# Performance work log

Hardware: AMD Instinct MI355X
Metric: run time of the kernel (lower is better)

## Reference

```python
import jax, jax.numpy as jnp
import numpy as np

B, SL, D, E, STEPS = 8, 1024, 128, 4, 5


def setup_inputs() -> dict:
    key = jax.random.key(0)
    ks = jax.random.split(key, 13)
    s = 0.02  # xavier-ish init scale
    return {
        "batchinput": jax.random.normal(ks[0], (B, SL, D), jnp.float32),
        # dense per-edge-type adjacency [B, sl, sl*E]; scaled so bmm output stays O(1)
        "batchgraphin": jax.random.uniform(ks[1], (B, SL, SL * E), jnp.float32) / SL,
        "batchgraphout": jax.random.uniform(ks[2], (B, SL, SL * E), jnp.float32) / SL,
        "W_in": jax.random.normal(ks[3], (E * D, E * D), jnp.float32) * s,
        "b_in": jnp.zeros((E * D,), jnp.float32),
        "W_out": jax.random.normal(ks[4], (E * D, E * D), jnp.float32) * s,
        "b_out": jnp.zeros((E * D,), jnp.float32),
        "W_r": jax.random.normal(ks[5], (D, 3 * D), jnp.float32) * s,
        "b_r": jnp.zeros((D,), jnp.float32),
        "W_z": jax.random.normal(ks[6], (D, 3 * D), jnp.float32) * s,
        "b_z": jnp.zeros((D,), jnp.float32),
        "W_t": jax.random.normal(ks[7], (D, 3 * D), jnp.float32) * s,
        "b_t": jnp.zeros((D,), jnp.float32),
    }


def reference(batchinput, batchgraphin, batchgraphout,
              W_in, b_in, W_out, b_out,
              W_r, b_r, W_z, b_z, W_t, b_t):
    out = batchinput  # [B, SL, D]
    for _ in range(STEPS):
        # tile node state across edge types: [B, SL, E*D]
        temp = jnp.broadcast_to(out[:, :, None, :], (B, SL, E, D)).reshape(B, SL, E * D)
        gi = (temp @ W_in.T + b_in).reshape(B, SL * E, D)
        gi = jnp.einsum('bse,bed->bsd', batchgraphin, gi)   # [B, SL, D]
        go = (temp @ W_out.T + b_out).reshape(B, SL * E, D)
        go = jnp.einsum('bse,bed->bsd', batchgraphout, go)  # [B, SL, D]
        # GRU-style gated update
        cat = jnp.concatenate([gi, go, out], axis=-1)       # [B, SL, 3D]
        r = jax.nn.sigmoid(cat @ W_r.T + b_r)
        z = jax.nn.sigmoid(cat @ W_z.T + b_z)
        h_hat = jnp.tanh(jnp.concatenate([gi, go, r * out], axis=-1) @ W_t.T + b_t)
        out = (1.0 - z) * out + z * h_hat
    return out
```

## Files before the change

### kernel.cpp

```cpp
#include <hip/hip_runtime.h>
#include <cstdint>
#include <cstddef>


typedef unsigned short u16;
typedef unsigned int u32;
typedef float f32x4 __attribute__((ext_vector_type(4)));
typedef short short8 __attribute__((ext_vector_type(8)));
typedef u16 u16x4 __attribute__((ext_vector_type(4)));
typedef u16 u16x8 __attribute__((ext_vector_type(8)));

__device__ __forceinline__ float b2f(u16 h) {
  union { u32 u; float f; } v; v.u = ((u32)h) << 16; return v.f;
}
__device__ __forceinline__ u16 f2bf(float f) {
  union { float f; u32 u; } v; v.f = f;
  u32 r = (v.u + 0x7fffu + ((v.u >> 16) & 1u)) >> 16;
  return (u16)r;
}
__device__ __forceinline__ float ldu(const void* p, size_t i, int flag) {
  return flag ? ((const float*)p)[i] : b2f(((const u16*)p)[i]);
}
__device__ __forceinline__ void gload_lds16(const void* g, void* l) {
  __builtin_amdgcn_global_load_lds((const __attribute__((address_space(1))) void*)g,
                                   (__attribute__((address_space(3))) void*)l,
                                   16, 0, 0);
}

__global__ void k_detect(const u16* g, int* flag) {
  __shared__ int bad;
  if (threadIdx.x == 0) bad = 0;
  __syncthreads();
  int any = 0;
  for (int i = threadIdx.x; i < 8192; i += 256) any |= (g[i] > 0x3B00);
  if (any) atomicOr(&bad, 1);
  __syncthreads();
  if (threadIdx.x == 0) *flag = bad;
}

__global__ void k_cvtf(const void* src, float* dst, int n, const int* flagp) {
  int i = blockIdx.x * 256 + threadIdx.x;
  if (i < n) dst[i] = ldu(src, i, *flagp);
}

__global__ void k_weff(const void* Win, const void* bin, const void* Wout, const void* bout,
                       u16* weffHT, u16* weffLT, float* biasf, const int* flagp) {
  int flag = *flagp;
  int idx = blockIdx.x * 256 + threadIdx.x;
  int j = idx >> 7, k = idx & 127;
  float s = 0.f;
  if (j < 512) {
#pragma unroll
    for (int e = 0; e < 4; e++) s += ldu(Win, (size_t)j * 512 + e * 128 + k, flag);
  } else {
#pragma unroll
    for (int e = 0; e < 4; e++) s += ldu(Wout, (size_t)(j - 512) * 512 + e * 128 + k, flag);
  }
  u16 h = f2bf(s);
  weffHT[(size_t)j * 128 + k] = h;
  weffLT[(size_t)j * 128 + k] = f2bf(s - b2f(h));
  if (idx < 1024) biasf[idx] = (idx < 512) ? ldu(bin, idx, flag) : ldu(bout, idx - 512, flag);
}

__global__ void k_wt3(const void* Wr, const void* Wz, const void* Wt,
                      const void* br, const void* bz, const void* bt,
                      u16* wt3H, u16* wt3L,
                      float* brf, float* bzf, float* btf, const int* flagp) {
  int flag = *flagp;
  int idx = blockIdx.x * 256 + threadIdx.x;
  int g = idx / 49152, rem = idx % 49152;
  const void* W = (g == 0) ? Wr : (g == 1) ? Wz : Wt;
  float s = ldu(W, rem, flag);
  u16 h = f2bf(s);
  wt3H[(size_t)idx] = h;
  wt3L[(size_t)idx] = f2bf(s - b2f(h));
  if (rem < 128) {
    float bv = ldu((g == 0) ? br : (g == 1) ? bz : bt, rem, flag);
    ((g == 0) ? brf : (g == 1) ? bzf : btf)[rem] = bv;
  }
}

__global__ __launch_bounds__(512, 2) void kg_pre_mfma(
    const u16* __restrict__ weffHT, const u16* __restrict__ weffLT,
    const float* __restrict__ biasf, const float* __restrict__ outF,
    u16* __restrict__ gpreT) {
  __shared__ __align__(16) u16 AH[32 * 128];
  __shared__ __align__(16) u16 AL[32 * 128];
  __shared__ __align__(16) u16 ybuf[32 * 1024];
  int t = threadIdx.x;
  int b = blockIdx.y;
  int s0 = blockIdx.x * 32;
  {
    int row = t >> 4, c8 = (t & 15) * 8;
    const float* src = outF + (((size_t)(b * 1024 + s0 + row)) << 7) + c8;
    f32x4 x0 = *(const f32x4*)src;
    f32x4 x1 = *(const f32x4*)(src + 4);
    u16x8 vh, vl;
#pragma unroll
    for (int i = 0; i < 4; i++) {
      float x = x0[i]; u16 h = f2bf(x);
      vh[i] = h; vl[i] = f2bf(x - b2f(h));
      x = x1[i]; h = f2bf(x);
      vh[i + 4] = h; vl[i + 4] = f2bf(x - b2f(h));
    }
    int bc = (c8 * 2) ^ ((row & 7) << 4);
    *(u16x8*)((char*)AH + row * 256 + bc) = vh;
    *(u16x8*)((char*)AL + row * 256 + bc) = vl;
  }
  __syncthreads();
  int lane = t & 63, w = t >> 6;
  int wm = w >> 2, wn = w & 3;
  int lr = lane & 15, lk = lane >> 4;
  int n0 = wn * 256;
  int arow = wm * 16 + lr;
  int abase_row = arow * 256;
  int aswz = (arow & 7) << 4;
  f32x4 acc[16] = {};
#pragma unroll
  for (int kk = 0; kk < 4; kk++) {
    int kb = (kk * 64 + lk * 16) ^ aswz;
    short8 ah = *(const short8*)((const char*)AH + abase_row + kb);
    short8 al = *(const short8*)((const char*)AL + abase_row + kb);
    int wko = kk * 64 + lk * 16;
#pragma unroll
    for (int nf = 0; nf < 16; nf++) {
      int j = n0 + nf * 16 + lr;
      short8 wh = *(const short8*)((const char*)weffHT + (size_t)j * 256 + wko);
      short8 wl = *(const short8*)((const char*)weffLT + (size_t)j * 256 + wko);
      acc[nf] = __builtin_amdgcn_mfma_f32_16x16x32_bf16(ah, wh, acc[nf], 0, 0, 0);
      acc[nf] = __builtin_amdgcn_mfma_f32_16x16x32_bf16(ah, wl, acc[nf], 0, 0, 0);
      acc[nf] = __builtin_amdgcn_mfma_f32_16x16x32_bf16(al, wh, acc[nf], 0, 0, 0);
    }
  }
#pragma unroll
  for (int nf = 0; nf < 16; nf++) {
    int j = n0 + nf * 16 + lr;
    float bj = biasf[j];
#pragma unroll
    for (int i = 0; i < 4; i++) {
      int s = wm * 16 + lk * 4 + i;
      ybuf[s * 1024 + j] = f2bf(acc[nf][i] + bj);
    }
  }
  __syncthreads();
#pragma unroll
  for (int p = 0; p < 8; p++) {
    int row = p * 32 + (t >> 4);
    int gate = row >> 7, d = row & 127;
    int c = (t & 15) * 8;
    u16x8 v;
#pragma unroll
    for (int i = 0; i < 8; i++) {
      int k2 = c + i;
      v[i] = ybuf[(k2 >> 2) * 1024 + gate * 512 + (k2 & 3) * 128 + d];
    }
    *(u16x8*)(gpreT + (((size_t)((gate * 8 + b) * 128 + d)) << 12) + (size_t)s0 * 4 + c) = v;
  }
}

template <int WMODE>
__global__ __launch_bounds__(256, 2) void kg_bmm(
    const void* __restrict__ gin, const void* __restrict__ gout,
    u16* __restrict__ gB, int useGB, int writeStep,
    const u16* __restrict__ gpreT,
    float* __restrict__ P,
    const int* __restrict__ flagp) {
  __shared__ __align__(16) u16 bufA[2][4096];
  __shared__ __align__(16) u16 bufB[2][8192];

  int t = threadIdx.x;
  int lin0 = blockIdx.x + (blockIdx.y << 4) + (blockIdx.z << 8);
  int lin = ((lin0 & 7) << 6) + (lin0 >> 3);
  int mb = lin & 15, gb = (lin >> 4) & 15, kh = lin >> 8;
  int gate = gb >> 3, b = gb & 7;
  int ms0 = mb << 6;
  int kbase = kh << 11;

  int flag = *flagp;
  int doWrite = 0, srcBF = 1;
  const void* Asrc;
  size_t abase;
  if (WMODE == 0) {
    if (flag) { Asrc = gB;                abase = (((size_t)(gb * 1024 + ms0)) << 12) + kbase; }
    else      { Asrc = gate ? gout : gin; abase = (((size_t)(b  * 1024 + ms0)) << 12) + kbase; }
  } else {
    doWrite = useGB && flag && writeStep;
    srcBF = (flag == 0);
    Asrc = gate ? gout : gin;
    abase = (((size_t)(b * 1024 + ms0)) << 12) + kbase;
  }
  size_t gwbase = (((size_t)(gb * 1024 + ms0)) << 12) + kbase;

  int arow = t >> 4;
  int acolE = (t & 15) << 2;
  int acb = (t & 15) << 3;
  int aswz = (arow & 7) << 4;
  int lane = t & 63, w = t >> 6;
  int wm = w >> 1, wn = w & 1;
  int lr = lane & 15, lk = lane >> 4;
  int r0 = wm * 32 + lr;
  int c0 = wn * 64 + lr;
  int fswz = (lr & 7) << 4;

  f32x4 acc[2][4] = {};
  f32x4 af[4]; u16x4 ah[4];

  auto stageA_load = [&](int st) {
    size_t kk = abase + (size_t)st * 64;
    if (WMODE == 0 || srcBF) {
      const u16* p = (const u16*)Asrc;
#pragma unroll
      for (int it = 0; it < 4; it++)
        ah[it] = *(const u16x4*)(p + kk + (size_t)(arow + it * 16) * 4096 + acolE);
    } else {
      const float* p = (const float*)Asrc;
#pragma unroll
      for (int it = 0; it < 4; it++) {
        const f32x4* a = (const f32x4*)(p + kk + (size_t)(arow + it * 16) * 4096 + acolE);
        af[it] = doWrite ? __builtin_nontemporal_load(a) : *a;
      }
    }
  };
  auto stageA_write = [&](int nb, int st) {
#pragma unroll
    for (int it = 0; it < 4; it++) {
      int row = arow + it * 16;
      u16x4 v;
      if (WMODE == 0 || srcBF) v = ah[it];
      else { v[0] = f2bf(af[it][0]); v[1] = f2bf(af[it][1]);
             v[2] = f2bf(af[it][2]); v[3] = f2bf(af[it][3]); }
      *(u16x4*)((char*)bufA[nb] + row * 128 + (acb ^ aswz)) = v;
      if (WMODE == 1 && doWrite)
        *(u16x4*)(gB + gwbase + (size_t)st * 64 + (size_t)row * 4096 + acolE) = v;
    }
  };
  auto stageB = [&](int st, int nb) {
    size_t kk = (size_t)kbase + (size_t)st * 64;
#pragma unroll
    for (int c = 0; c < 4; c++) {
      int col = (w << 5) + (c << 3) + (lane >> 3);
      int j = (lane & 7) ^ (col & 7);
      const u16* g = gpreT + (((size_t)(gb * 128 + col)) << 12) + kk + (size_t)j * 8;
      u16* l = &bufB[nb][w * 2048 + c * 512];
      gload_lds16(g, l);
    }
  };
  auto compute = [&](int cur) {
    const char* A = (const char*)bufA[cur];
    const char* B = (const char*)bufB[cur];
#pragma unroll
    for (int ks = 0; ks < 2; ks++) {
      int kb = (ks * 64 + lk * 16) ^ fswz;
      short8 a0 = *(const short8*)(A + r0 * 128 + kb);
      short8 a1 = *(const short8*)(A + r0 * 128 + 2048 + kb);
#pragma unroll
      for (int nf = 0; nf < 4; nf++) {
        short8 bv = *(const short8*)(B + c0 * 128 + nf * 2048 + kb);
        acc[0][nf] = __builtin_amdgcn_mfma_f32_16x16x32_bf16(a0, bv, acc[0][nf], 0, 0, 0);
        acc[1][nf] = __builtin_amdgcn_mfma_f32_16x16x32_bf16(a1, bv, acc[1][nf], 0, 0, 0);
      }
    }
  };

  stageA_load(0);
  stageB(0, 0);
  stageA_write(0, 0);
  __syncthreads();
  int cur = 0;
#pragma unroll 2
  for (int st = 0; st < 32; st++) {
    if (st < 31) { stageA_load(st + 1); stageB(st + 1, cur ^ 1); }
    compute(cur);
    if (st < 31) stageA_write(cur ^ 1, st + 1);
    __syncthreads();
    cur ^= 1;
  }

  float* Pp = P + (((size_t)(kh * 16 + gb)) << 17);
#pragma unroll
  for (int mf = 0; mf < 2; mf++) {
#pragma unroll
    for (int nf = 0; nf < 4; nf++) {
      int rowb = ms0 + wm * 32 + mf * 16 + lk * 4;
      int col = wn * 64 + nf * 16 + lr;
#pragma unroll
      for (int j = 0; j < 4; j++)
        Pp[(size_t)(rowb + j) * 128 + col] = acc[mf][nf][j];
    }
  }
}

__global__ __launch_bounds__(256, 2) void kg_gate_mfma(
    const float* __restrict__ P, float* __restrict__ outF,
    const u16* __restrict__ wt3H, const u16* __restrict__ wt3L,
    const float* __restrict__ brf, const float* __restrict__ bzf,
    const float* __restrict__ btf,
    const int* __restrict__ flagp, void* __restrict__ dout, int writeOut) {
  __shared__ __align__(16) u16 csH[16 * 384];
  __shared__ __align__(16) u16 csL[16 * 384];
  __shared__ __align__(16) float outS[16 * 128];
  __shared__ __align__(16) float zs[16 * 128];
  __shared__ __align__(16) u16 rsH[16 * 128];
  __shared__ __align__(16) u16 rsL[16 * 128];
  int t = threadIdx.x;
  int m0 = blockIdx.x * 16;
  int b = m0 >> 10;
  for (int i4 = t; i4 < 1536; i4 += 256) {
    int r = i4 / 96, q = i4 % 96;
    int m = m0 + r, s = m & 1023;
    f32x4 v;
    if (q < 64) {
      int gate = q >> 5;
      size_t idx = (((size_t)(gate * 8 + b)) << 17) + ((size_t)s << 7) + ((size_t)(q & 31) << 2);
      v = *(const f32x4*)(P + idx) + *(const f32x4*)(P + ((size_t)1 << 21) + idx);
    } else {
      v = *(const f32x4*)(outF + ((size_t)m << 7) + ((q - 64) << 2));
      *(f32x4*)&outS[r * 128 + ((q - 64) << 2)] = v;
    }
    u16x4 vh, vl;
#pragma unroll
    for (int i = 0; i < 4; i++) {
      u16 h = f2bf(v[i]);
      vh[i] = h; vl[i] = f2bf(v[i] - b2f(h));
    }
    int byte = (q * 8) ^ ((r & 7) << 4);
    *(u16x4*)((char*)csH + r * 768 + byte) = vh;
    *(u16x4*)((char*)csL + r * 768 + byte) = vl;
  }
  __syncthreads();

  int lane = t & 63, w = t >> 6;
  int lr = lane & 15, lk = lane >> 4;
  int aswz = (lr & 7) << 4;
  const char* cH = (const char*)csH + lr * 768;
  const char* cL = (const char*)csL + lr * 768;
  f32x4 accR[2] = {}, accZ[2] = {}, accT[2] = {};
  for (int kc = 0; kc < 12; kc++) {
    int ab = (kc * 64 + lk * 16) ^ aswz;
    short8 aH = *(const short8*)(cH + ab);
    short8 aL = *(const short8*)(cL + ab);
    int kb = kc * 64 + lk * 16;
#pragma unroll
    for (int nf = 0; nf < 2; nf++) {
      int nl = w * 32 + nf * 16 + lr;
      size_t offR = (size_t)nl * 768 + kb;
      size_t offZ = (size_t)(128 + nl) * 768 + kb;
      short8 bH = *(const short8*)((const char*)wt3H + offR);
      short8 bL = *(const short8*)((const char*)wt3L + offR);
      accR[nf] = __builtin_amdgcn_mfma_f32_16x16x32_bf16(aH, bH, accR[nf], 0, 0, 0);
      accR[nf] = __builtin_amdgcn_mfma_f32_16x16x32_bf16(aH, bL, accR[nf], 0, 0, 0);
      accR[nf] = __builtin_amdgcn_mfma_f32_16x16x32_bf16(aL, bH, accR[nf], 0, 0, 0);
      bH = *(const short8*)((const char*)wt3H + offZ);
      bL = *(const short8*)((const char*)wt3L + offZ);
      accZ[nf] = __builtin_amdgcn_mfma_f32_16x16x32_bf16(aH, bH, accZ[nf], 0, 0, 0);
      accZ[nf] = __builtin_amdgcn_mfma_f32_16x16x32_bf16(aH, bL, accZ[nf], 0, 0, 0);
      accZ[nf] = __builtin_amdgcn_mfma_f32_16x16x32_bf16(aL, bH, accZ[nf], 0, 0, 0);
      if (kc < 8) {
        size_t offT = (size_t)(256 + nl) * 768 + kb;
        bH = *(const short8*)((const char*)wt3H + offT);
        bL = *(const short8*)((const char*)wt3L + offT);
        accT[nf] = __builtin_amdgcn_mfma_f32_16x16x32_bf16(aH, bH, accT[nf], 0, 0, 0);
        accT[nf] = __builtin_amdgcn_mfma_f32_16x16x32_bf16(aH, bL, accT[nf], 0, 0, 0);
        accT[nf] = __builtin_amdgcn_mfma_f32_16x16x32_bf16(aL, bH, accT[nf], 0, 0, 0);
      }
    }
  }
#pragma unroll
  for (int nf = 0; nf < 2; nf++) {
    int nl = w * 32 + nf * 16 + lr;
    float bR = brf[nl], bZ = bzf[nl];
#pragma unroll
    for (int i = 0; i < 4; i++) {
      int row = lk * 4 + i;
      float rv = 1.f / (1.f + __expf(-(accR[nf][i] + bR)));
      float zv = 1.f / (1.f + __expf(-(accZ[nf][i] + bZ)));
      zs[row * 128 + nl] = zv;
      float rp = rv * outS[row * 128 + nl];
      u16 h = f2bf(rp);
      int byte = (nl * 2) ^ ((row & 7) << 4);
      *(u16*)((char*)rsH + row * 256 + byte) = h;
      *(u16*)((char*)rsL + row * 256 + byte) = f2bf(rp - b2f(h));
    }
  }
  __syncthreads();
  const char* rH = (const char*)rsH + lr * 256;
  const char* rL = (const char*)rsL + lr * 256;
#pragma unroll
  for (int kc = 0; kc < 4; kc++) {
    int ab = (kc * 64 + lk * 16) ^ aswz;
    short8 aH = *(const short8*)(rH + ab);
    short8 aL = *(const short8*)(rL + ab);
    int kb = 512 + kc * 64 + lk * 16;
#pragma unroll
    for (int nf = 0; nf < 2; nf++) {
      int nl = w * 32 + nf * 16 + lr;
      size_t off = (size_t)(256 + nl) * 768 + kb;
      short8 bH = *(const short8*)((const char*)wt3H + off);
      short8 bL = *(const short8*)((const char*)wt3L + off);
      accT[nf] = __builtin_amdgcn_mfma_f32_16x16x32_bf16(aH, bH, accT[nf], 0, 0, 0);
      accT[nf] = __builtin_amdgcn_mfma_f32_16x16x32_bf16(aH, bL, accT[nf], 0, 0, 0);
      accT[nf] = __builtin_amdgcn_mfma_f32_16x16x32_bf16(aL, bH, accT[nf], 0, 0, 0);
    }
  }
  int flag = *flagp;
#pragma unroll
  for (int nf = 0; nf < 2; nf++) {
    int nl = w * 32 + nf * 16 + lr;
    float bT = btf[nl];
#pragma unroll
    for (int i = 0; i < 4; i++) {
      int row = lk * 4 + i;
      float h = tanhf(accT[nf][i] + bT);
      float z = zs[row * 128 + nl];
      float ov = outS[row * 128 + nl];
      float res = (1.f - z) * ov + z * h;
      size_t o = (size_t)(m0 + row) * 128 + nl;
      outF[o] = res;
      if (writeOut) {
        if (flag) ((float*)dout)[o] = res;
        else      ((u16*)dout)[o] = f2bf(res);
      }
    }
  }
}

extern "C" void kernel_launch(void* const* d_in, const int* in_sizes, int n_in,
                              void* d_out, int out_size, void* d_ws, size_t ws_size,
                              hipStream_t stream) {
  const void* X    = d_in[0];
  const void* Gin  = d_in[1];
  const void* Gout = d_in[2];
  const void* Win  = d_in[3];
  const void* bin  = d_in[4];
  const void* Wout = d_in[5];
  const void* bout = d_in[6];
  const void* Wr   = d_in[7];
  const void* br   = d_in[8];
  const void* Wz   = d_in[9];
  const void* bz   = d_in[10];
  const void* Wt   = d_in[11];
  const void* bt   = d_in[12];

  char* w = (char*)d_ws;
  auto alloc = [&](size_t n) { char* p = w; w += (n + 255) & ~(size_t)255; return p; };
  int*   flag    = (int*)alloc(4);
  u16*   weffHT  = (u16*)alloc((size_t)1024 * 128 * 2);
  u16*   weffLT  = (u16*)alloc((size_t)1024 * 128 * 2);
  float* biasf   = (float*)alloc(1024 * 4);
  u16*   wt3H    = (u16*)alloc((size_t)3 * 128 * 384 * 2);
  u16*   wt3L    = (u16*)alloc((size_t)3 * 128 * 384 * 2);
  float* brf     = (float*)alloc(128 * 4);
  float* bzf     = (float*)alloc(128 * 4);
  float* btf     = (float*)alloc(128 * 4);
  float* outF    = (float*)alloc((size_t)8192 * 128 * 4);
  u16*   gpreT   = (u16*)alloc((size_t)16 * 128 * 4096 * 2);
  float* partial = (float*)alloc((size_t)2 * 16 * 1024 * 128 * 4);
  u16*   gB      = (u16*)alloc((size_t)2 * 8 * 1024 * 4096 * 2);
  int wsok = ((size_t)(w - (char*)d_ws) <= ws_size) ? 1 : 0;
  (void)in_sizes; (void)n_in; (void)out_size;

  k_detect<<<1, 256, 0, stream>>>((const u16*)Gin, flag);
  k_weff<<<512, 256, 0, stream>>>(Win, bin, Wout, bout, weffHT, weffLT, biasf, flag);
  k_wt3<<<576, 256, 0, stream>>>(Wr, Wz, Wt, br, bz, bt, wt3H, wt3L, brf, bzf, btf, flag);
  k_cvtf<<<4096, 256, 0, stream>>>(X, outF, 1048576, flag);

  for (int step = 0; step < 5; step++) {
    kg_pre_mfma<<<dim3(32, 8), 512, 0, stream>>>(weffHT, weffLT, biasf, outF, gpreT);
    if (step == 0 || !wsok)
      kg_bmm<1><<<dim3(16, 16, 2), 256, 0, stream>>>(Gin, Gout, gB, wsok,
                                                     (step == 0) ? 1 : 0,
                                                     gpreT, partial, flag);
    else
      kg_bmm<0><<<dim3(16, 16, 2), 256, 0, stream>>>(Gin, Gout, gB, wsok, 0,
                                                     gpreT, partial, flag);
    kg_gate_mfma<<<512, 256, 0, stream>>>(partial, outF, wt3H, wt3L, brf, bzf, btf,
                                          flag, d_out, (step == 4) ? 1 : 0);
  }
}
```

Measured before the change: 892.4 us.

## Fuse next-step pre-projection GEMM into gate kernel epilogue

The gate kernel now also computes the next step's edge-type projection (out @ Weff) for its 16 rows with MFMA, using split bf16 hi/lo, and writes the transposed gpreT directly. This removes the separate kg_pre_mfma launch for steps 1-4 and the round trip of the new state through global memory. Shared memory is reorganized into one aliased buffer, and z is kept in registers instead of LDS. The risk is extra register pressure and lower occupancy in the gate kernel, plus a heavier per-block epilogue that now streams weff from global memory in every block.

```diff
diff --git a/kernel.cpp b/kernel.cpp
--- a/kernel.cpp
+++ b/kernel.cpp
@@ -290,18 +290,25 @@
   }
 }
 
+template <int DOPRE>
 __global__ __launch_bounds__(256, 2) void kg_gate_mfma(
     const float* __restrict__ P, float* __restrict__ outF,
     const u16* __restrict__ wt3H, const u16* __restrict__ wt3L,
+    const u16* __restrict__ weffHT, const u16* __restrict__ weffLT,
     const float* __restrict__ brf, const float* __restrict__ bzf,
-    const float* __restrict__ btf,
+    const float* __restrict__ btf, const float* __restrict__ biasf,
+    u16* __restrict__ gpreT,
     const int* __restrict__ flagp, void* __restrict__ dout, int writeOut) {
-  __shared__ __align__(16) u16 csH[16 * 384];
-  __shared__ __align__(16) u16 csL[16 * 384];
-  __shared__ __align__(16) float outS[16 * 128];
-  __shared__ __align__(16) float zs[16 * 128];
-  __shared__ __align__(16) u16 rsH[16 * 128];
-  __shared__ __align__(16) u16 rsL[16 * 128];
+  __shared__ __align__(16) char smem[40960];
+  u16* csH   = (u16*)(smem);
+  u16* csL   = (u16*)(smem + 12288);
+  u16* rsH   = (u16*)(smem + 24576);
+  u16* rsL   = (u16*)(smem + 28672);
+  float* outS = (float*)(smem + 32768);
+  u16* ybuf  = (u16*)(smem);
+  u16* resH  = (u16*)(smem + 32768);
+  u16* resL  = (u16*)(smem + 36864);
+
   int t = threadIdx.x;
   int m0 = blockIdx.x * 16;
   int b = m0 >> 10;
@@ -365,6 +372,7 @@
       }
     }
   }
+  float zreg[2][4];
 #pragma unroll
   for (int nf = 0; nf < 2; nf++) {
     int nl = w * 32 + nf * 16 + lr;
@@ -373,8 +381,7 @@
     for (int i = 0; i < 4; i++) {
       int row = lk * 4 + i;
       float rv = 1.f / (1.f + __expf(-(accR[nf][i] + bR)));
-      float zv = 1.f / (1.f + __expf(-(accZ[nf][i] + bZ)));
-      zs[row * 128 + nl] = zv;
+      zreg[nf][i] = 1.f / (1.f + __expf(-(accZ[nf][i] + bZ)));
       float rp = rv * outS[row * 128 + nl];
       u16 h = f2bf(rp);
       int byte = (nl * 2) ^ ((row & 7) << 4);
@@ -403,6 +410,7 @@
     }
   }
   int flag = *flagp;
+  float resv[2][4];
 #pragma unroll
   for (int nf = 0; nf < 2; nf++) {
     int nl = w * 32 + nf * 16 + lr;
@@ -411,14 +419,76 @@
     for (int i = 0; i < 4; i++) {
       int row = lk * 4 + i;
       float h = tanhf(accT[nf][i] + bT);
-      float z = zs[row * 128 + nl];
+      float z = zreg[nf][i];
       float ov = outS[row * 128 + nl];
       float res = (1.f - z) * ov + z * h;
+      resv[nf][i] = res;
       size_t o = (size_t)(m0 + row) * 128 + nl;
       outF[o] = res;
       if (writeOut) {
         if (flag) ((float*)dout)[o] = res;
         else      ((u16*)dout)[o] = f2bf(res);
+      }
+    }
+  }
+  if (DOPRE) {
+    __syncthreads();
+#pragma unroll
+    for (int nf = 0; nf < 2; nf++) {
+      int nl = w * 32 + nf * 16 + lr;
+#pragma unroll
+      for (int i = 0; i < 4; i++) {
+        int row = lk * 4 + i;
+        float x = resv[nf][i];
+        u16 h = f2bf(x);
+        int byte = (nl * 2) ^ ((row & 7) << 4);
+        *(u16*)((char*)resH + row * 256 + byte) = h;
+        *(u16*)((char*)resL + row * 256 + byte) = f2bf(x - b2f(h));
+      }
+    }
+    __syncthreads();
+    f32x4 pacc[16] = {};
+#pragma unroll
+    for (int kk = 0; kk < 4; kk++) {
+      int kb = (kk * 64 + lk * 16) ^ aswz;
+      short8 ah = *(const short8*)((const char*)resH + lr * 256 + kb);
+      short8 al = *(const short8*)((const char*)resL + lr * 256 + kb);
+      int wko = kk * 64 + lk * 16;
+#pragma unroll
+      for (int nf = 0; nf < 16; nf++) {
+        int j = w * 256 + nf * 16 + lr;
+        short8 wh = *(const short8*)((const char*)weffHT + (size_t)j * 256 + wko);
+        short8 wl = *(const short8*)((const char*)weffLT + (size_t)j * 256 + wko);
+        pacc[nf] = __builtin_amdgcn_mfma_f32_16x16x32_bf16(ah, wh, pacc[nf], 0, 0, 0);
+        pacc[nf] = __builtin_amdgcn_mfma_f32_16x16x32_bf16(ah, wl, pacc[nf], 0, 0, 0);
+        pacc[nf] = __builtin_amdgcn_mfma_f32_16x16x32_bf16(al, wh, pacc[nf], 0, 0, 0);
+      }
+    }
+#pragma unroll
+    for (int nf = 0; nf < 16; nf++) {
+      int j = w * 256 + nf * 16 + lr;
+      float bj = biasf[j];
+#pragma unroll
+      for (int i = 0; i < 4; i++) {
+        int s = lk * 4 + i;
+        ybuf[s * 1024 + j] = f2bf(pacc[nf][i] + bj);
+      }
+    }
+    __syncthreads();
+    {
+      int row = t;
+      int gate = row >> 7, d = row & 127;
+      int sbase = (m0 & 1023) * 4;
+      u16* op = gpreT + (((size_t)((gate * 8 + b) * 128 + d)) << 12) + sbase;
+#pragma unroll
+      for (int p = 0; p < 8; p++) {
+        u16x8 v;
+#pragma unroll
+        for (int i = 0; i < 8; i++) {
+          int k2 = p * 8 + i;
+          v[i] = ybuf[(k2 >> 2) * 1024 + gate * 512 + (k2 & 3) * 128 + d];
+        }
+        *(u16x8*)(op + p * 8) = v;
       }
     }
   }
@@ -464,8 +534,8 @@
   k_wt3<<<576, 256, 0, stream>>>(Wr, Wz, Wt, br, bz, bt, wt3H, wt3L, brf, bzf, btf, flag);
   k_cvtf<<<4096, 256, 0, stream>>>(X, outF, 1048576, flag);
 
+  kg_pre_mfma<<<dim3(32, 8), 512, 0, stream>>>(weffHT, weffLT, biasf, outF, gpreT);
   for (int step = 0; step < 5; step++) {
-    kg_pre_mfma<<<dim3(32, 8), 512, 0, stream>>>(weffHT, weffLT, biasf, outF, gpreT);
     if (step == 0 || !wsok)
       kg_bmm<1><<<dim3(16, 16, 2), 256, 0, stream>>>(Gin, Gout, gB, wsok,
                                                      (step == 0) ? 1 : 0,
@@ -473,7 +543,13 @@
     else
       kg_bmm<0><<<dim3(16, 16, 2), 256, 0, stream>>>(Gin, Gout, gB, wsok, 0,
                                                      gpreT, partial, flag);
-    kg_gate_mfma<<<512, 256, 0, stream>>>(partial, outF, wt3H, wt3L, brf, bzf, btf,
-                                          flag, d_out, (step == 4) ? 1 : 0);
-  }
-}
+    if (step < 4)
+      kg_gate_mfma<1><<<512, 256, 0, stream>>>(partial, outF, wt3H, wt3L,
+                                               weffHT, weffLT, brf, bzf, btf, biasf,
+                                               gpreT, flag, d_out, 0);
+    else
+      kg_gate_mfma<0><<<512, 256, 0, stream>>>(partial, outF, wt3H, wt3L,
+                                               weffHT, weffLT, brf, bzf, btf, biasf,
+                                               gpreT, flag, d_out, 1);
+  }
+}
```

New measurement: 885.1 us. About the same (-0.8%).
